# Performance work log

Measured on AMD Instinct MI355X. Metric: run time of the kernel, lower is better.

## Reference

```python
import jax, jax.numpy as jnp
import numpy as np

N, F, HID, OUT, H = 4096, 128, 64, 16, 4
ALPHA = 0.2          # leaky relu slope
NEG = -9e15          # mask fill value (pyGAT convention)


def setup_inputs() -> dict:
    key = jax.random.key(0)
    ks = jax.random.split(key, 8)
    x = jax.random.normal(ks[0], (N, F), dtype=jnp.float32)
    adj = jax.random.randint(ks[1], (N, N), 0, 2, dtype=jnp.int32)
    s = lambda *sh: 0.1
    W_in = jax.random.normal(ks[2], (H, F, F), dtype=jnp.float32) * 0.1
    a_in = jax.random.normal(ks[3], (H, 2 * F), dtype=jnp.float32) * 0.1
    W_hid = jax.random.normal(ks[4], (H, F * H, HID), dtype=jnp.float32) * 0.1
    a_hid = jax.random.normal(ks[5], (H, 2 * HID), dtype=jnp.float32) * 0.1
    W_out = jax.random.normal(ks[6], (HID * H, OUT), dtype=jnp.float32) * 0.1
    a_out = jax.random.normal(ks[7], (2 * OUT,), dtype=jnp.float32) * 0.1
    return {"x": x, "adj": adj, "W_in": W_in, "a_in": a_in,
            "W_hid": W_hid, "a_hid": a_hid, "W_out": W_out, "a_out": a_out}


def _multi_head_att(x, W, a, mask):
    """Dense multi-head GAT aggregation. x:[N,Fin], W:[H,Fin,D], a:[H,2D] -> [H,N,D]."""
    D = W.shape[-1]
    h = jnp.einsum('nf,hfd->hnd', x, W)                      # [H,N,D]
    f1 = jnp.einsum('hnd,hd->hn', h, a[:, :D])               # source scores
    f2 = jnp.einsum('hnd,hd->hn', h, a[:, D:])               # target scores
    e = jax.nn.leaky_relu(f1[:, :, None] + f2[:, None, :], ALPHA)  # [H,N,N]
    e = jnp.where(mask[None, :, :], e, NEG)
    att = jax.nn.softmax(e, axis=-1)
    return jnp.einsum('hnm,hmd->hnd', att, h)                # [H,N,D]


def _concat_heads(h):
    # [H,N,D] -> [N,H*D]
    Hh, n, d = h.shape
    return jnp.transpose(h, (1, 0, 2)).reshape(n, Hh * d)


def reference(x, adj, W_in, a_in, W_hid, a_hid, W_out, a_out):
    mask = adj > 0
    # input attention block: concat=True (ELU per head), identity skip (in==out dim)
    h1 = _multi_head_att(x, W_in, a_in, mask)                # [H,N,F]
    h1 = jax.nn.elu(h1 + x[None, :, :])                      # identity residual
    h1 = _concat_heads(h1)                                   # [N,H*F]
    # hidden attention block: concat=True
    h2 = _multi_head_att(h1, W_hid, a_hid, mask)             # [H,N,HID]
    h2 = _concat_heads(jax.nn.elu(h2))                       # [N,H*HID]
    # output attention layer: single head, concat=False (no ELU inside)
    h3 = _multi_head_att(h2, W_out[None], a_out[None], mask)[0]  # [N,OUT]
    return jax.nn.log_softmax(jax.nn.elu(h3), axis=1)
```

## Files before the change

kernel.cpp:

```cpp
#include <hip/hip_runtime.h>
#include <math.h>

#define NN 4096
#define FF 128
#define HH 4
#define HIDD 64
#define OUTD 16
#define MASKW (NN / 32)
#define ALPHA 0.2f

typedef __attribute__((ext_vector_type(8))) short short8;
typedef __attribute__((ext_vector_type(4))) float f32x4;

__device__ __forceinline__ ushort f2bf(float f) {
    unsigned u = __float_as_uint(f);
    return (ushort)((u + 0x7fffu + ((u >> 16) & 1u)) >> 16);
}
__device__ __forceinline__ float bf2f(ushort u) {
    return __uint_as_float((unsigned)u << 16);
}

__global__ void pack_mask_kernel(const int* __restrict__ adj, unsigned int* __restrict__ mb) {
    int t = blockIdx.x * 256 + threadIdx.x;
    int v = adj[t] > 0;
    unsigned long long bal = __ballot(v);
    if ((threadIdx.x & 63) == 0) {
        int w = t >> 5;
        mb[w] = (unsigned int)(bal & 0xffffffffULL);
        mb[w + 1] = (unsigned int)(bal >> 32);
    }
}

__global__ void cvt_kernel(const float* __restrict__ x, ushort* __restrict__ xb) {
    int e = (blockIdx.x * 256 + threadIdx.x) * 4;
    f32x4 v = *(const f32x4*)&x[e];
    unsigned lo = (unsigned)f2bf(v[0]) | ((unsigned)f2bf(v[1]) << 16);
    unsigned hi = (unsigned)f2bf(v[2]) | ((unsigned)f2bf(v[3]) << 16);
    uint2 p; p.x = lo; p.y = hi;
    *(uint2*)&xb[e] = p;
}

__global__ void wtprep_kernel(const float* __restrict__ W_in, const float* __restrict__ W_hid,
                              const float* __restrict__ W_out,
                              ushort* __restrict__ wt1, ushort* __restrict__ wt2,
                              ushort* __restrict__ wt3) {
    int idx = blockIdx.x * 256 + threadIdx.x;
    if (idx < 65536) {
        int k = idx & 127, n = (idx >> 7) & 127, hd = idx >> 14;
        wt1[idx] = f2bf(W_in[((size_t)hd * 128 + k) * 128 + n]);
    } else if (idx < 65536 + 131072) {
        int j = idx - 65536;
        int k = j & 511, n = (j >> 9) & 63, hd = j >> 15;
        wt2[j] = f2bf(W_hid[((size_t)hd * 512 + k) * 64 + n]);
    } else if (idx < 65536 + 131072 + 4096) {
        int j = idx - 196608;
        int k = j & 255, n = j >> 8;
        wt3[j] = f2bf(W_out[(size_t)k * 16 + n]);
    }
}

__global__ void vprep_kernel(const float* __restrict__ W_in, const float* __restrict__ a_in,
                             const float* __restrict__ W_hid, const float* __restrict__ a_hid,
                             const float* __restrict__ W_out, const float* __restrict__ a_out,
                             float* __restrict__ vbuf) {
    int idx = blockIdx.x * 256 + threadIdx.x;
    const float* Wr; const float* ar; int D; float* dst;
    if (idx < 1024) {
        int f = idx & 127, hd = (idx >> 7) & 3, s = idx >> 9;
        Wr = W_in + ((size_t)hd * 128 + f) * 128;
        ar = a_in + hd * 256 + s * 128;
        D = 128; dst = &vbuf[idx];
    } else if (idx < 1024 + 4096) {
        int j = idx - 1024;
        int f = j & 511, hd = (j >> 9) & 3, s = j >> 11;
        Wr = W_hid + ((size_t)hd * 512 + f) * 64;
        ar = a_hid + hd * 128 + s * 64;
        D = 64; dst = &vbuf[1024 + j];
    } else if (idx < 1024 + 4096 + 512) {
        int j = idx - 5120;
        int f = j & 255, s = j >> 8;
        Wr = W_out + (size_t)f * 16;
        ar = a_out + s * 16;
        D = 16; dst = &vbuf[5120 + j];
    } else return;
    float s = 0.f;
    for (int d = 0; d < D; d++) s += Wr[d] * ar[d];
    *dst = s;
}

template <typename T, int K, int H>
__global__ __launch_bounds__(256) void score_kernel(const T* __restrict__ A,
                                                    const float* __restrict__ v,
                                                    float* __restrict__ f1,
                                                    float* __restrict__ f2) {
    int wv = blockIdx.x * 4 + (threadIdx.x >> 6);
    int lane = threadIdx.x & 63;
    int hd = wv >> 12;
    int i = wv & (NN - 1);
    const T* ar = A + (size_t)i * K;
    const float* v1r = v + (size_t)hd * K;
    const float* v2r = v + (size_t)(H + hd) * K;
    float s1 = 0.f, s2 = 0.f;
    for (int f = lane; f < K; f += 64) {
        float av;
        if constexpr (sizeof(T) == 2) av = bf2f(((const ushort*)ar)[f]);
        else av = ((const float*)ar)[f];
        s1 += av * v1r[f];
        s2 += av * v2r[f];
    }
#pragma unroll
    for (int o = 32; o > 0; o >>= 1) {
        s1 += __shfl_down(s1, o);
        s2 += __shfl_down(s2, o);
    }
    if (lane == 0) { f1[wv] = s1; f2[wv] = s2; }
}

__global__ void gmax_kernel(const float* __restrict__ f2, float* __restrict__ gmax) {
    int hd = blockIdx.x;
    const float* p = f2 + (size_t)hd * NN;
    float m = -1e30f;
    for (int i = threadIdx.x; i < NN; i += 256) m = fmaxf(m, p[i]);
    __shared__ float sm[4];
#pragma unroll
    for (int off = 32; off > 0; off >>= 1) m = fmaxf(m, __shfl_down(m, off));
    if ((threadIdx.x & 63) == 0) sm[threadIdx.x >> 6] = m;
    __syncthreads();
    if (threadIdx.x == 0) gmax[hd] = fmaxf(fmaxf(sm[0], sm[1]), fmaxf(sm[2], sm[3]));
}

template <int K, int N, int CFG>
__global__ __launch_bounds__(256) void proj_mfma_kernel(const ushort* __restrict__ A,
                                                        const ushort* __restrict__ WT,
                                                        ushort* __restrict__ hT) {
    constexpr int NT = (CFG == 0) ? (N / 64) : (N / 16);
    __shared__ ushort ts[4][NT * 16][20];
    const int hd = blockIdx.y;
    const int t = threadIdx.x;
    const int w = t >> 6, lane = t & 63, ln = lane & 15, g = lane >> 4, g8 = g * 8;
    const int i0 = (CFG == 0) ? blockIdx.x * 16 : blockIdx.x * 64 + w * 16;
    const int n0 = (CFG == 0) ? w * (N / 4) : 0;
    const ushort* WTh = WT + (size_t)hd * N * K;
    ushort* hTh = hT + (size_t)hd * N * NN;
    f32x4 acc[NT];
#pragma unroll
    for (int n = 0; n < NT; n++) acc[n] = (f32x4)(0.f);
    const ushort* arow = A + (size_t)(i0 + ln) * K + g8;
#pragma unroll
    for (int k0 = 0; k0 < K; k0 += 32) {
        short8 aF = *(const short8*)&arow[k0];
#pragma unroll
        for (int n = 0; n < NT; n++) {
            short8 bF = *(const short8*)&WTh[(size_t)(n0 + n * 16 + ln) * K + k0 + g8];
            acc[n] = __builtin_amdgcn_mfma_f32_16x16x32_bf16(aF, bF, acc[n], 0, 0, 0);
        }
    }
#pragma unroll
    for (int n = 0; n < NT; n++) {
        unsigned lo = (unsigned)f2bf(acc[n][0]) | ((unsigned)f2bf(acc[n][1]) << 16);
        unsigned hi = (unsigned)f2bf(acc[n][2]) | ((unsigned)f2bf(acc[n][3]) << 16);
        uint2 p; p.x = lo; p.y = hi;
        *(uint2*)&ts[w][n * 16 + ln][g * 4] = p;
    }
#pragma unroll
    for (int n = 0; n < NT; n++) {
        int d = lane >> 2, ip = lane & 3;
        uint2 rv = *(uint2*)&ts[w][n * 16 + d][ip * 4];
        *(uint2*)&hTh[(size_t)(n0 + n * 16 + d) * NN + i0 + ip * 4] = rv;
    }
}

template <int D>
__global__ __launch_bounds__(256) void agg7_kernel(const ushort* __restrict__ hT,
                                                   const float* __restrict__ f1,
                                                   const float* __restrict__ f2,
                                                   const float* __restrict__ gmax,
                                                   const unsigned int* __restrict__ mb,
                                                   float* __restrict__ pacc,
                                                   float* __restrict__ plsum) {
    constexpr int NT = D / 16;
    constexpr int CHS = NT * 64;
    constexpr int NC = NT / 2;
    __shared__ ushort hs[2 * CHS * 8];
    const int hd = blockIdx.z;
    const int js = blockIdx.y;
    const int jlen = NN / gridDim.y;
    const int jb = js * jlen, je = jb + jlen;
    const int combo = js * HH + hd;

    const int t = threadIdx.x;
    const int w = t >> 6;
    const int lane = t & 63;
    const int ln = lane & 15;
    const int g = lane >> 4;
    const int g8 = g * 8;
    const int i0 = blockIdx.x * 64 + w * 16;
    const ushort* hTh = hT + (size_t)hd * D * NN;

    const float f1v = f1[hd * NN + i0 + ln];
    const float gm = gmax[hd];
    float mi = f1v + gm;
    mi = fmaxf(mi, ALPHA * mi);
    const float L2E = 1.442695040888963f;
    const float cexp = -mi * L2E;

    f32x4 acc[NT];
#pragma unroll
    for (int n = 0; n < NT; n++) acc[n] = (f32x4)(0.f);
    f32x4 accl = (f32x4)(0.f);
    short8 bONE;
#pragma unroll
    for (int q = 0; q < 8; q++) bONE[q] = (short)0x3F80;

    const float* f2h = f2 + hd * NN;
    const unsigned* mrow = mb + (size_t)(i0 + ln) * MASKW;

    int srow[NC], scol[NC], soff[NC];
#pragma unroll
    for (int c = 0; c < NC; c++) {
        int ch = t + c * 256;
        int s = ch / CHS;
        int inner = ch - s * CHS;
        int n = inner >> 6;
        int l = inner & 63;
        srow[c] = n * 16 + (l & 15);
        scol[c] = s * 32 + (l >> 4) * 8;
        soff[c] = ch * 8;
    }
    uint4 st[NC];
#pragma unroll
    for (int c = 0; c < NC; c++)
        st[c] = *(const uint4*)&hTh[(size_t)srow[c] * NN + jb + scol[c]];

    for (int j0 = jb; j0 < je; j0 += 64) {
        __syncthreads();
#pragma unroll
        for (int c = 0; c < NC; c++) *(uint4*)&hs[soff[c]] = st[c];
        __syncthreads();
        const bool more = (j0 + 64) < je;
        if (more) {
#pragma unroll
            for (int c = 0; c < NC; c++)
                st[c] = *(const uint4*)&hTh[(size_t)srow[c] * NN + j0 + 64 + scol[c]];
        }
        uint2 mw2 = *(const uint2*)&mrow[j0 >> 5];
#pragma unroll
        for (int s = 0; s < 2; s++) {
            unsigned bits = ((s ? mw2.y : mw2.x) >> g8) & 0xffu;
            f32x4 cA = *(const f32x4*)&f2h[j0 + s * 32 + g8];
            f32x4 cB = *(const f32x4*)&f2h[j0 + s * 32 + g8 + 4];
            unsigned au[4];
#pragma unroll
            for (int tp = 0; tp < 4; tp++) {
                unsigned pu[2];
#pragma unroll
                for (int q = 0; q < 2; q++) {
                    int tt = tp * 2 + q;
                    float f2t = (tt < 4) ? cA[tt] : cB[tt - 4];
                    float e = f1v + f2t;
                    e = fmaxf(e, ALPHA * e);
                    float p = ((bits >> tt) & 1u) ? __builtin_amdgcn_exp2f(e * L2E + cexp) : 0.f;
                    pu[q] = __float_as_uint(p) & 0xffff0000u;
                }
                au[tp] = (pu[0] >> 16) | pu[1];
            }
            union { unsigned u[4]; short8 v; } aF;
#pragma unroll
            for (int q = 0; q < 4; q++) aF.u[q] = au[q];
#pragma unroll
            for (int n = 0; n < NT; n++) {
                short8 bF = *(const short8*)&hs[((s * NT + n) * 64 + lane) * 8];
                acc[n] = __builtin_amdgcn_mfma_f32_16x16x32_bf16(aF.v, bF, acc[n], 0, 0, 0);
            }
            accl = __builtin_amdgcn_mfma_f32_16x16x32_bf16(aF.v, bONE, accl, 0, 0, 0);
        }
    }
    if (ln == 0) {
#pragma unroll
        for (int r = 0; r < 4; r++)
            plsum[(size_t)combo * NN + i0 + g * 4 + r] = accl[r];
    }
    float* pb = pacc + (size_t)combo * NN * D;
#pragma unroll
    for (int n = 0; n < NT; n++) {
#pragma unroll
        for (int r = 0; r < 4; r++) {
            pb[(size_t)(i0 + g * 4 + r) * D + n * 16 + ln] = acc[n][r];
        }
    }
}

template <int D, int EPI>
__global__ __launch_bounds__(256) void combine_kernel(const float* __restrict__ pacc,
                                                      const float* __restrict__ plsum,
                                                      const float* __restrict__ xres,
                                                      ushort* __restrict__ out,
                                                      int ncols, int JS) {
    const int hd = blockIdx.y;
    const int e = (blockIdx.x * 256 + threadIdx.x) * 4;
    const int row = e / D;
    const int col = e % D;
    f32x4 s = (f32x4)(0.f);
    float l = 0.f;
    for (int js = 0; js < JS; js++) {
        const size_t cix = (size_t)(js * HH + hd) * NN;
        s += *(const f32x4*)&pacc[(cix + row) * D + col];
        l += plsum[cix + row];
    }
    const float inv = 1.f / l;
    f32x4 xv;
    if (EPI == 1) xv = *(const f32x4*)&xres[(size_t)row * D + col];
    float o[4];
#pragma unroll
    for (int k = 0; k < 4; k++) {
        float v = s[k] * inv;
        if (EPI == 1) v += xv[k];
        if (EPI >= 1) v = v > 0.f ? v : (__expf(v) - 1.f);
        o[k] = v;
    }
    unsigned lo = (unsigned)f2bf(o[0]) | ((unsigned)f2bf(o[1]) << 16);
    unsigned hi = (unsigned)f2bf(o[2]) | ((unsigned)f2bf(o[3]) << 16);
    uint2 p; p.x = lo; p.y = hi;
    *(uint2*)&out[(size_t)row * ncols + hd * D + col] = p;
}

template <int D, int EPI, int NW>
__global__ __launch_bounds__(NW * 64) void agg_mfma_kernel(const ushort* __restrict__ hT,
                                                           const float* __restrict__ f1,
                                                           const float* __restrict__ f2,
                                                           const float* __restrict__ gmax,
                                                           const unsigned int* __restrict__ mb,
                                                           const float* __restrict__ xres,
                                                           float* __restrict__ out, int ncols) {
    constexpr int NT = D / 16;
    static_assert(NW == 1 || NT == 1, "j-split only for single-tile D");
    const int hd = blockIdx.z;
    const int i0 = blockIdx.x * 16;
    const int w = threadIdx.x >> 6;
    const int lane = threadIdx.x & 63;
    const int ln = lane & 15;
    const int g = lane >> 4;
    const int g8 = g * 8;
    const ushort* hTh = hT + (size_t)hd * D * NN;
    const float f1v = f1[hd * NN + i0 + ln];
    const float gm = gmax[hd];
    float mi = f1v + gm;
    mi = fmaxf(mi, ALPHA * mi);
    f32x4 acc[NT];
#pragma unroll
    for (int n = 0; n < NT; n++) acc[n] = (f32x4)(0.f);
    float lsum = 0.f;
    const float* f2h = f2 + hd * NN;
    const unsigned* mrow = mb + (size_t)(i0 + ln) * MASKW;
    const int jbeg = w * (NN / NW), jend = jbeg + NN / NW;

    for (int j0 = jbeg; j0 < jend; j0 += 32) {
        unsigned bits = (mrow[j0 >> 5] >> g8) & 0xffu;
        f32x4 fA = *(const f32x4*)&f2h[j0 + g8];
        f32x4 fB = *(const f32x4*)&f2h[j0 + g8 + 4];
        short8 aF;
#pragma unroll
        for (int t = 0; t < 8; t++) {
            float f2t = (t < 4) ? fA[t] : fB[t - 4];
            float e = f1v + f2t;
            e = fmaxf(e, ALPHA * e);
            float p = ((bits >> t) & 1u) ? __expf(e - mi) : 0.f;
            ushort pb = f2bf(p);
            aF[t] = (short)pb;
            lsum += __uint_as_float((unsigned)pb << 16);
        }
#pragma unroll
        for (int n = 0; n < NT; n++) {
            short8 bF = *(const short8*)&hTh[(size_t)(n * 16 + ln) * NN + j0 + g8];
            acc[n] = __builtin_amdgcn_mfma_f32_16x16x32_bf16(aF, bF, acc[n], 0, 0, 0);
        }
    }
    lsum += __shfl_xor(lsum, 16);
    lsum += __shfl_xor(lsum, 32);

    float accF[NT][4];
    float ltot;
    __shared__ float accL[NW][16][17];
    __shared__ float lsL[NW][16];
    if constexpr (NW == 1) {
#pragma unroll
        for (int n = 0; n < NT; n++)
#pragma unroll
            for (int r = 0; r < 4; r++) accF[n][r] = acc[n][r];
        ltot = lsum;
    } else {
#pragma unroll
        for (int r = 0; r < 4; r++) accL[w][g * 4 + r][ln] = acc[0][r];
        if (lane < 16) lsL[w][lane] = lsum;
        __syncthreads();
        if (w != 0) return;
#pragma unroll
        for (int r = 0; r < 4; r++) {
            float s = 0.f;
            for (int ww = 0; ww < NW; ww++) s += accL[ww][g * 4 + r][ln];
            accF[0][r] = s;
        }
        float s = 0.f;
        for (int ww = 0; ww < NW; ww++) s += lsL[ww][ln];
        ltot = s;
    }
    const float linv = 1.f / ltot;
#pragma unroll
    for (int n = 0; n < NT; n++) {
#pragma unroll
        for (int r = 0; r < 4; r++) {
            float invr = __shfl(linv, (g << 2) + r);
            float v = accF[n][r] * invr;
            int row = i0 + g * 4 + r;
            int col = n * 16 + ln;
            if (EPI == 1) v += xres[(size_t)row * D + col];
            if (EPI >= 1) v = v > 0.f ? v : (__expf(v) - 1.f);
            out[(size_t)row * ncols + hd * D + col] = v;
        }
    }
}

__global__ void final_kernel(const float* __restrict__ h3, float* __restrict__ out) {
    int i = blockIdx.x * 256 + threadIdx.x;
    if (i >= NN) return;
    float v[OUTD];
    float mx = -1e30f;
#pragma unroll
    for (int k = 0; k < OUTD; k++) {
        float e = h3[(size_t)i * OUTD + k];
        e = e > 0.f ? e : (__expf(e) - 1.f);
        v[k] = e;
        mx = fmaxf(mx, e);
    }
    float s = 0.f;
#pragma unroll
    for (int k = 0; k < OUTD; k++) s += __expf(v[k] - mx);
    float ls = logf(s);
#pragma unroll
    for (int k = 0; k < OUTD; k++) out[(size_t)i * OUTD + k] = v[k] - mx - ls;
}

extern "C" void kernel_launch(void* const* d_in, const int* in_sizes, int n_in,
                              void* d_out, int out_size, void* d_ws, size_t ws_size,
                              hipStream_t stream) {
    const float* x = (const float*)d_in[0];
    const int* adj = (const int*)d_in[1];
    const float* W_in = (const float*)d_in[2];
    const float* a_in = (const float*)d_in[3];
    const float* W_hid = (const float*)d_in[4];
    const float* a_hid = (const float*)d_in[5];
    const float* W_out = (const float*)d_in[6];
    const float* a_out = (const float*)d_in[7];
    float* out = (float*)d_out;

    char* w = (char*)d_ws;
    unsigned int* mb = (unsigned int*)w;  w += (size_t)NN * MASKW * 4;
    ushort* hT = (ushort*)w;              w += (size_t)HH * NN * FF * 2;
    ushort* xb16 = (ushort*)w;            w += (size_t)NN * FF * 2;
    ushort* cat1b = (ushort*)w;           w += (size_t)NN * (HH * FF) * 2;
    ushort* cat2b = (ushort*)w;           w += (size_t)NN * (HH * HIDD) * 2;
    ushort* wt1 = (ushort*)w;             w += 65536 * 2;
    ushort* wt2 = (ushort*)w;             w += 131072 * 2;
    ushort* wt3 = (ushort*)w;             w += 4096 * 2;
    float* vbuf = (float*)w;              w += 5632 * 4;
    float* f1 = (float*)w;                w += (size_t)HH * NN * 4;
    float* f2 = (float*)w;                w += (size_t)HH * NN * 4;
    float* gm = (float*)w;                w += 256;
    float* h3 = (float*)w;                w += (size_t)NN * OUTD * 4;
    size_t base_used = (size_t)(w - (char*)d_ws);

    int lgJS = -1;
    float* pacc = (float*)w;
    float* plsum = nullptr;
    {
        size_t per_js = (size_t)HH * NN * FF * 4;
        size_t ls_bytes = (size_t)32 * NN * 4;
        for (int lg = 2; lg >= 0; lg--) {
            size_t cand = (size_t)1 << lg;
            size_t need = base_used + cand * per_js + ls_bytes + 1024;
            if (ws_size >= need) { lgJS = lg; break; }
        }
        if (lgJS >= 0) plsum = (float*)((char*)pacc + ((size_t)1 << lgJS) * per_js);
    }
    const int JS = (lgJS >= 0) ? (1 << lgJS) : 1;
    const int JS2 = (lgJS >= 0) ? 2 * JS : 1;

    hipLaunchKernelGGL(pack_mask_kernel, dim3(NN * NN / 256), dim3(256), 0, stream, adj, mb);
    hipLaunchKernelGGL(cvt_kernel, dim3(NN * FF / 1024), dim3(256), 0, stream, x, xb16);
    hipLaunchKernelGGL(wtprep_kernel, dim3(784), dim3(256), 0, stream,
                       W_in, W_hid, W_out, wt1, wt2, wt3);
    hipLaunchKernelGGL(vprep_kernel, dim3(22), dim3(256), 0, stream,
                       W_in, a_in, W_hid, a_hid, W_out, a_out, vbuf);

    hipLaunchKernelGGL((proj_mfma_kernel<FF, FF, 0>), dim3(NN / 16, HH), dim3(256), 0, stream,
                       xb16, wt1, hT);
    hipLaunchKernelGGL((score_kernel<float, FF, HH>), dim3(HH * NN / 4), dim3(256), 0, stream,
                       x, vbuf, f1, f2);
    hipLaunchKernelGGL(gmax_kernel, dim3(HH), dim3(256), 0, stream, f2, gm);
    hipLaunchKernelGGL((agg7_kernel<FF>), dim3(NN / 64, JS, HH), dim3(256), 0, stream,
                       hT, f1, f2, gm, mb, pacc, plsum);
    hipLaunchKernelGGL((combine_kernel<FF, 1>), dim3(NN * FF / 1024, HH), dim3(256), 0, stream,
                       pacc, plsum, x, cat1b, HH * FF, JS);

    hipLaunchKernelGGL((proj_mfma_kernel<HH * FF, HIDD, 0>), dim3(NN / 16, HH), dim3(256), 0, stream,
                       cat1b, wt2, hT);
    hipLaunchKernelGGL((score_kernel<ushort, HH * FF, HH>), dim3(HH * NN / 4), dim3(256), 0, stream,
                       cat1b, vbuf + 1024, f1, f2);
    hipLaunchKernelGGL(gmax_kernel, dim3(HH), dim3(256), 0, stream, f2, gm);
    hipLaunchKernelGGL((agg7_kernel<HIDD>), dim3(NN / 64, JS2, HH), dim3(256), 0, stream,
                       hT, f1, f2, gm, mb, pacc, plsum);
    hipLaunchKernelGGL((combine_kernel<HIDD, 2>), dim3(NN * HIDD / 1024, HH), dim3(256), 0, stream,
                       pacc, plsum, (const float*)nullptr, cat2b, HH * HIDD, JS2);

    hipLaunchKernelGGL((proj_mfma_kernel<HH * HIDD, OUTD, 1>), dim3(NN / 64, 1), dim3(256), 0, stream,
                       cat2b, wt3, hT);
    hipLaunchKernelGGL((score_kernel<ushort, HH * HIDD, 1>), dim3(NN / 4), dim3(256), 0, stream,
                       cat2b, vbuf + 5120, f1, f2);
    hipLaunchKernelGGL(gmax_kernel, dim3(1), dim3(256), 0, stream, f2, gm);
    hipLaunchKernelGGL((agg_mfma_kernel<OUTD, 0, 4>), dim3(NN / 16, 1, 1), dim3(256), 0, stream,
                       hT, f1, f2, gm, mb, (const float*)nullptr, h3, OUTD);

    hipLaunchKernelGGL(final_kernel, dim3(NN / 256), dim3(256), 0, stream, h3, out);
}
```

Before: 412.1 us.

## Switch aggregation to 32-wide tiles with padded LDS and scalar row sums

Replaces the aggregation kernel with a variant that processes 32 neighbor columns per step using a padded row-major shared-memory tile. The mask word and target scores are prefetched one step ahead. The softmax denominator is accumulated with scalar adds and cross-lane shuffles instead of an extra MFMA against a ones vector. This cuts one MFMA per step and simplifies staging, but doubles the number of barriers. The padded LDS stride may also misalign the 16-byte fragment reads.

```diff
diff --git a/kernel.cpp b/kernel.cpp
--- a/kernel.cpp
+++ b/kernel.cpp
@@ -171,7 +171,7 @@
 }
 
 template <int D>
-__global__ __launch_bounds__(256) void agg7_kernel(const ushort* __restrict__ hT,
+__global__ __launch_bounds__(256) void agg3_kernel(const ushort* __restrict__ hT,
                                                    const float* __restrict__ f1,
                                                    const float* __restrict__ f2,
                                                    const float* __restrict__ gmax,
@@ -179,15 +179,12 @@
                                                    float* __restrict__ pacc,
                                                    float* __restrict__ plsum) {
     constexpr int NT = D / 16;
-    constexpr int CHS = NT * 64;
-    constexpr int NC = NT / 2;
-    __shared__ ushort hs[2 * CHS * 8];
+    constexpr int NC = D / 64;
+    __shared__ ushort hs[D][34];
     const int hd = blockIdx.z;
     const int js = blockIdx.y;
     const int jlen = NN / gridDim.y;
     const int jb = js * jlen, je = jb + jlen;
-    const int combo = js * HH + hd;
-
     const int t = threadIdx.x;
     const int w = t >> 6;
     const int lane = t & 63;
@@ -207,80 +204,73 @@
     f32x4 acc[NT];
 #pragma unroll
     for (int n = 0; n < NT; n++) acc[n] = (f32x4)(0.f);
-    f32x4 accl = (f32x4)(0.f);
-    short8 bONE;
-#pragma unroll
-    for (int q = 0; q < 8; q++) bONE[q] = (short)0x3F80;
-
+    float lsum = 0.f;
     const float* f2h = f2 + hd * NN;
     const unsigned* mrow = mb + (size_t)(i0 + ln) * MASKW;
 
-    int srow[NC], scol[NC], soff[NC];
+    int srow[NC], scol[NC];
 #pragma unroll
     for (int c = 0; c < NC; c++) {
         int ch = t + c * 256;
-        int s = ch / CHS;
-        int inner = ch - s * CHS;
-        int n = inner >> 6;
-        int l = inner & 63;
-        srow[c] = n * 16 + (l & 15);
-        scol[c] = s * 32 + (l >> 4) * 8;
-        soff[c] = ch * 8;
+        srow[c] = ch >> 2;
+        scol[c] = (ch & 3) * 8;
     }
     uint4 st[NC];
 #pragma unroll
     for (int c = 0; c < NC; c++)
         st[c] = *(const uint4*)&hTh[(size_t)srow[c] * NN + jb + scol[c]];
-
-    for (int j0 = jb; j0 < je; j0 += 64) {
+    unsigned mw = mrow[jb >> 5];
+    f32x4 fA = *(const f32x4*)&f2h[jb + g8];
+    f32x4 fB = *(const f32x4*)&f2h[jb + g8 + 4];
+
+    for (int j0 = jb; j0 < je; j0 += 32) {
         __syncthreads();
 #pragma unroll
-        for (int c = 0; c < NC; c++) *(uint4*)&hs[soff[c]] = st[c];
+        for (int c = 0; c < NC; c++) *(uint4*)&hs[srow[c]][scol[c]] = st[c];
         __syncthreads();
-        const bool more = (j0 + 64) < je;
+        const bool more = (j0 + 32) < je;
         if (more) {
 #pragma unroll
             for (int c = 0; c < NC; c++)
-                st[c] = *(const uint4*)&hTh[(size_t)srow[c] * NN + j0 + 64 + scol[c]];
-        }
-        uint2 mw2 = *(const uint2*)&mrow[j0 >> 5];
-#pragma unroll
-        for (int s = 0; s < 2; s++) {
-            unsigned bits = ((s ? mw2.y : mw2.x) >> g8) & 0xffu;
-            f32x4 cA = *(const f32x4*)&f2h[j0 + s * 32 + g8];
-            f32x4 cB = *(const f32x4*)&f2h[j0 + s * 32 + g8 + 4];
-            unsigned au[4];
-#pragma unroll
-            for (int tp = 0; tp < 4; tp++) {
-                unsigned pu[2];
-#pragma unroll
-                for (int q = 0; q < 2; q++) {
-                    int tt = tp * 2 + q;
-                    float f2t = (tt < 4) ? cA[tt] : cB[tt - 4];
-                    float e = f1v + f2t;
-                    e = fmaxf(e, ALPHA * e);
-                    float p = ((bits >> tt) & 1u) ? __builtin_amdgcn_exp2f(e * L2E + cexp) : 0.f;
-                    pu[q] = __float_as_uint(p) & 0xffff0000u;
-                }
-                au[tp] = (pu[0] >> 16) | pu[1];
+                st[c] = *(const uint4*)&hTh[(size_t)srow[c] * NN + j0 + 32 + scol[c]];
+        }
+        unsigned bits = (mw >> g8) & 0xffu;
+        f32x4 cA = fA, cB = fB;
+        if (more) {
+            mw = mrow[(j0 + 32) >> 5];
+            fA = *(const f32x4*)&f2h[j0 + 32 + g8];
+            fB = *(const f32x4*)&f2h[j0 + 32 + g8 + 4];
+        }
+        unsigned au[4];
+#pragma unroll
+        for (int tp = 0; tp < 4; tp++) {
+            unsigned pu[2];
+#pragma unroll
+            for (int q = 0; q < 2; q++) {
+                int tt = tp * 2 + q;
+                float f2t = (tt < 4) ? cA[tt] : cB[tt - 4];
+                float e = f1v + f2t;
+                e = fmaxf(e, ALPHA * e);
+                float p = ((bits >> tt) & 1u) ? __builtin_amdgcn_exp2f(e * L2E + cexp) : 0.f;
+                pu[q] = __float_as_uint(p) & 0xffff0000u;
+                lsum += __uint_as_float(pu[q]);
             }
-            union { unsigned u[4]; short8 v; } aF;
-#pragma unroll
-            for (int q = 0; q < 4; q++) aF.u[q] = au[q];
-#pragma unroll
-            for (int n = 0; n < NT; n++) {
-                short8 bF = *(const short8*)&hs[((s * NT + n) * 64 + lane) * 8];
-                acc[n] = __builtin_amdgcn_mfma_f32_16x16x32_bf16(aF.v, bF, acc[n], 0, 0, 0);
-            }
-            accl = __builtin_amdgcn_mfma_f32_16x16x32_bf16(aF.v, bONE, accl, 0, 0, 0);
-        }
-    }
-    if (ln == 0) {
-#pragma unroll
-        for (int r = 0; r < 4; r++)
-            plsum[(size_t)combo * NN + i0 + g * 4 + r] = accl[r];
-    }
-    float* pb = pacc + (size_t)combo * NN * D;
+            au[tp] = (pu[0] >> 16) | pu[1];
+        }
+        union { unsigned u[4]; short8 s; } aF;
+#pragma unroll
+        for (int q = 0; q < 4; q++) aF.u[q] = au[q];
+#pragma unroll
+        for (int n = 0; n < NT; n++) {
+            short8 bF = *(const short8*)&hs[n * 16 + ln][g8];
+            acc[n] = __builtin_amdgcn_mfma_f32_16x16x32_bf16(aF.s, bF, acc[n], 0, 0, 0);
+        }
+    }
+    lsum += __shfl_xor(lsum, 16);
+    lsum += __shfl_xor(lsum, 32);
+    const size_t pbase = ((size_t)js * HH + hd) * NN;
+    if (g == 0) plsum[pbase + i0 + ln] = lsum;
+    float* pb = pacc + pbase * D;
 #pragma unroll
     for (int n = 0; n < NT; n++) {
 #pragma unroll
@@ -303,9 +293,9 @@
     f32x4 s = (f32x4)(0.f);
     float l = 0.f;
     for (int js = 0; js < JS; js++) {
-        const size_t cix = (size_t)(js * HH + hd) * NN;
-        s += *(const f32x4*)&pacc[(cix + row) * D + col];
-        l += plsum[cix + row];
+        const size_t pbase = ((size_t)js * HH + hd) * NN;
+        s += *(const f32x4*)&pacc[(pbase + row) * D + col];
+        l += plsum[pbase + row];
     }
     const float inv = 1.f / l;
     f32x4 xv;
@@ -497,7 +487,7 @@
     hipLaunchKernelGGL((score_kernel<float, FF, HH>), dim3(HH * NN / 4), dim3(256), 0, stream,
                        x, vbuf, f1, f2);
     hipLaunchKernelGGL(gmax_kernel, dim3(HH), dim3(256), 0, stream, f2, gm);
-    hipLaunchKernelGGL((agg7_kernel<FF>), dim3(NN / 64, JS, HH), dim3(256), 0, stream,
+    hipLaunchKernelGGL((agg3_kernel<FF>), dim3(NN / 64, JS, HH), dim3(256), 0, stream,
                        hT, f1, f2, gm, mb, pacc, plsum);
     hipLaunchKernelGGL((combine_kernel<FF, 1>), dim3(NN * FF / 1024, HH), dim3(256), 0, stream,
                        pacc, plsum, x, cat1b, HH * FF, JS);
@@ -507,7 +497,7 @@
     hipLaunchKernelGGL((score_kernel<ushort, HH * FF, HH>), dim3(HH * NN / 4), dim3(256), 0, stream,
                        cat1b, vbuf + 1024, f1, f2);
     hipLaunchKernelGGL(gmax_kernel, dim3(HH), dim3(256), 0, stream, f2, gm);
-    hipLaunchKernelGGL((agg7_kernel<HIDD>), dim3(NN / 64, JS2, HH), dim3(256), 0, stream,
+    hipLaunchKernelGGL((agg3_kernel<HIDD>), dim3(NN / 64, JS2, HH), dim3(256), 0, stream,
                        hT, f1, f2, gm, mb, pacc, plsum);
     hipLaunchKernelGGL((combine_kernel<HIDD, 2>), dim3(NN * HIDD / 1024, HH), dim3(256), 0, stream,
                        pacc, plsum, (const float*)nullptr, cat2b, HH * HIDD, JS2);
```

After: 379.4 us. -7.9%, faster.
